# Optimization experiments

Hardware: AMD Instinct MI355X
Metric: run time of the kernel (lower is better)

The kernel has to match this reference:

```python
import math
import jax, jax.numpy as jnp
import numpy as np

B, T, HID = 8, 2048, 1536
H, D = 8, 192
CHUNK, PAST, FUT = 12, 12, 0
CTX = CHUNK + PAST + FUT          # 24
F = PAST + FUT + 1                # 13 relative positions
CAP = 50.0
INVALID = -1.0e9


def setup_inputs() -> dict:
    key = jax.random.key(0)
    k1, k2, k3 = jax.random.split(key, 3)
    x = jax.random.normal(k1, (B, T, HID), dtype=jnp.float32)
    mask = jnp.zeros((B, T), dtype=bool)  # True = invalid/padding
    # causal validity: key offset (c - PAST) relative to query w must lie in [-PAST, FUT]
    w = jnp.arange(CHUNK)[:, None]
    c = jnp.arange(CTX)[None, :]
    causal_valid_mask = (c >= w) & (c <= w + PAST + FUT)  # [CHUNK, CTX]
    W_qkv = jax.random.normal(k2, (HID, 3 * HID), dtype=jnp.float32) * 0.02
    W_pos = jax.random.normal(k3, (HID, HID), dtype=jnp.float32) * 0.02
    per_dim_scale = jnp.zeros((D,), dtype=jnp.float32)
    return {"x": x, "mask": mask, "causal_valid_mask": causal_valid_mask,
            "W_qkv": W_qkv, "W_pos": W_pos, "per_dim_scale": per_dim_scale}


def _extract_block_context(z, U):
    # pad time dim left=PAST, right=FUT+CHUNK-1, then frame with step CHUNK, len CTX
    pad = ((0, 0), (PAST, FUT + CHUNK - 1)) + ((0, 0),) * (z.ndim - 2)
    zp = jnp.pad(z, pad)
    idx = jnp.arange(U)[:, None] * CHUNK + jnp.arange(CTX)[None, :]  # [U, CTX]
    return zp[:, idx]  # [B, U, CTX, ...]


def reference(x, mask, causal_valid_mask, W_qkv, W_pos, per_dim_scale):
    b, t, _ = x.shape
    qkv = x @ W_qkv
    q, k, v = jnp.split(qkv, 3, axis=-1)
    q = q.reshape(b, t, H, D)
    k = k.reshape(b, t, H, D)
    v = v.reshape(b, t, H, D)

    q_scale = D ** (-0.5) / math.log(2.0)
    k_scale = math.log(1.0 + math.e) / math.log(2.0)
    q = q * q_scale * jax.nn.softplus(per_dim_scale)  # per-dim scale on queries
    k = k * k_scale

    U = -(-t // CHUNK)  # ceil
    pad_q = U * CHUNK - t
    qb = jnp.pad(q, ((0, 0), (0, pad_q), (0, 0), (0, 0))).reshape(b, U, CHUNK, H, D)
    kb = _extract_block_context(k, U)            # [B,U,CTX,H,D]
    vb = _extract_block_context(v, U)            # [B,U,CTX,H,D]
    valid = _extract_block_context(~mask, U)     # [B,U,CTX]

    # ---- relative position embedding (Transformer-XL style) ----
    pos = jnp.arange(PAST, -FUT - 1, -1, dtype=jnp.float32)  # [F]
    nts = HID // 2
    inv_ts = jnp.exp(jnp.arange(nts, dtype=jnp.float32) * (-(math.log(10000.0) / (nts - 1))))
    st = pos[:, None] * inv_ts[None, :]
    emb = jnp.concatenate([jnp.sin(st), jnp.cos(st)], axis=-1)  # [F, HID]
    sin_emb = (emb @ W_pos).reshape(F, H, D)

    term_ac = jnp.einsum('buwhd,buchd->bhuwc', qb, kb)     # content-content
    term_bd = jnp.einsum('buwhd,fhd->bhuwf', qb, sin_emb)  # content-position
    # relative shift: pad last dim to CTX+1, flatten, slice, reshape
    pad_amt = CTX + 1 - F
    tb = jnp.pad(term_bd, ((0, 0),) * 4 + ((0, pad_amt),))
    tb = tb.reshape(b, H, U, CHUNK * (CTX + 1))[..., :CHUNK * CTX]
    tb = tb.reshape(b, H, U, CHUNK, CTX)

    logits = term_ac + tb
    logits = jnp.tanh(logits / CAP) * CAP  # softcap
    cond = valid[:, None, :, None, :] & causal_valid_mask[None, None, None, :, :]
    logits = jnp.where(cond, logits, INVALID)
    probs = jax.nn.softmax(logits, axis=-1)
    out = jnp.einsum('bhuwc,buchd->buwhd', probs, vb)
    return out.reshape(b, U * CHUNK, H, D)[:, :t]
```

## Files before the change

kernel.cpp:

```cpp
#include <hip/hip_runtime.h>

typedef unsigned int u32;
typedef unsigned short u16;

typedef __attribute__((ext_vector_type(8))) short bf16x8;
typedef __attribute__((ext_vector_type(4))) float f32x4;

__device__ __forceinline__ u16 f2bf(float f) {
  u32 u = __builtin_bit_cast(u32, f);
  u32 r = (u + 0x7fffu + ((u >> 16) & 1u)) >> 16;
  return (u16)r;
}
__device__ __forceinline__ float bfl(u32 u) { return __builtin_bit_cast(float, u << 16); }
__device__ __forceinline__ float bfh(u32 u) { return __builtin_bit_cast(float, u & 0xffff0000u); }

__device__ __forceinline__ void gload_lds16(const u16* g, u16* l) {
  __builtin_amdgcn_global_load_lds(
      (const __attribute__((address_space(1))) void*)g,
      (__attribute__((address_space(3))) void*)l, 16, 0, 0);
}

__global__ __launch_bounds__(256) void transp_wt(const float* __restrict__ W,
                                                 u16* __restrict__ Wt) {
  __shared__ float tile[64][68];
  int bk = blockIdx.x % 24, bn = blockIdx.x / 24;
  int k0 = bk * 64, n0 = bn * 64;
  int tid = threadIdx.x;
#pragma unroll
  for (int p = 0; p < 4; p++) {
    int idx = p * 256 + tid;
    int r = idx >> 4, c4 = idx & 15;
    *(float4*)&tile[r][c4 * 4] = *(const float4*)&W[(size_t)(k0 + r) * 4608 + n0 + c4 * 4];
  }
  __syncthreads();
#pragma unroll
  for (int p = 0; p < 2; p++) {
    int idx = p * 256 + tid;
    int rn = idx >> 3, kc = idx & 7;
    u16 pk[8];
#pragma unroll
    for (int e = 0; e < 8; e++) pk[e] = f2bf(tile[kc * 8 + e][rn]);
    *(uint4*)&Wt[(size_t)(n0 + rn) * 1536 + k0 + kc * 8] = *(const uint4*)pk;
  }
}

__global__ __launch_bounds__(256) void conv_x(const float* __restrict__ X,
                                              u16* __restrict__ Xb) {
  int i = blockIdx.x * 256 + threadIdx.x;
  const float4* xp = (const float4*)X;
  float4 a = xp[i * 2], b = xp[i * 2 + 1];
  uint4 o;
  o.x = (u32)f2bf(a.x) | ((u32)f2bf(a.y) << 16);
  o.y = (u32)f2bf(a.z) | ((u32)f2bf(a.w) << 16);
  o.z = (u32)f2bf(b.x) | ((u32)f2bf(b.y) << 16);
  o.w = (u32)f2bf(b.z) | ((u32)f2bf(b.w) << 16);
  ((uint4*)Xb)[i] = o;
}

__global__ __launch_bounds__(256) void pos_emb_part(const float* __restrict__ Wp,
                                                    float* __restrict__ part) {
  __shared__ float er[13 * 32];
  int ks = blockIdx.x % 48, nb = blockIdx.x / 48;
  int tid = threadIdx.x;
  int n = nb * 256 + tid;
  const float cfreq = 9.210340371976184f / 767.0f;
  for (int i = tid; i < 13 * 32; i += 256) {
    int f = i >> 5, kk = i & 31;
    int k = ks * 32 + kk;
    int ii = (k < 768) ? k : (k - 768);
    float fr = expf(-cfreq * (float)ii);
    float st = (float)(12 - f) * fr;
    er[f * 32 + kk] = (k < 768) ? sinf(st) : cosf(st);
  }
  __syncthreads();
  float acc[13];
#pragma unroll
  for (int f = 0; f < 13; f++) acc[f] = 0.f;
  const float* wp = Wp + (size_t)(ks * 32) * 1536 + n;
  for (int kk = 0; kk < 32; kk++) {
    float w = wp[(size_t)kk * 1536];
#pragma unroll
    for (int f = 0; f < 13; f++) acc[f] = fmaf(er[f * 32 + kk], w, acc[f]);
  }
#pragma unroll
  for (int f = 0; f < 13; f++)
    part[((size_t)ks * 13 + f) * 1536 + n] = acc[f];
}

__global__ __launch_bounds__(256) void pos_emb_red(const float* __restrict__ part,
                                                   u16* __restrict__ sembbf) {
  int idxg = blockIdx.x * 256 + threadIdx.x;
  int f = idxg / 1536, n = idxg % 1536;
  float s = 0.f;
  if (f < 13)
    for (int ks = 0; ks < 48; ks++)
      s += part[((size_t)ks * 13 + f) * 1536 + n];
  sembbf[idxg] = f2bf(s);
}

__global__ __launch_bounds__(512, 2) void gemm_qkv(const u16* __restrict__ Xb,
                                                   const u16* __restrict__ Bt,
                                                   u16* __restrict__ C,
                                                   const float* __restrict__ pds) {
  extern __shared__ u16 smem[];

  const int tid = threadIdx.x;
  const int lane = tid & 63;
  const int wv = tid >> 6;
  const int wr = wv >> 2;
  const int wc = wv & 3;
  const int lr = lane & 15;
  const int lkq = lane >> 4;
  const int sx = lr & 7;

  int bid = blockIdx.x;
  int xcd = bid & 7, idx = bid >> 3;
  int bm = xcd * 8 + idx / 24;
  int bn = idx % 24;
  int m0 = bm * 256, n0 = bn * 192;

  auto stageA = [&](int T) {
#pragma unroll
    for (int q = 0; q < 4; q++) {
      int ch = q * 512 + tid;
      int r = ch >> 3, cr = ch & 7;
      int crs = cr ^ (r & 7);
      const u16* g = Xb + (size_t)(m0 + r) * 1536 + T * 64 + crs * 8;
      u16* l = smem + (T % 3) * 16384 + ch * 8;
      gload_lds16(g, l);
    }
  };
  auto stageB = [&](int T) {
#pragma unroll
    for (int q = 0; q < 3; q++) {
      int ch = q * 512 + tid;
      int r = ch >> 3, cr = ch & 7;
      int crs = cr ^ (r & 7);
      const u16* g = Bt + (size_t)(n0 + r) * 1536 + T * 64 + crs * 8;
      u16* l = smem + 49152 + (T & 1) * 12288 + ch * 8;
      gload_lds16(g, l);
    }
  };

  f32x4 acc[8][3];
#pragma unroll
  for (int i = 0; i < 8; i++)
#pragma unroll
    for (int j = 0; j < 3; j++) acc[i][j] = (f32x4){0.f, 0.f, 0.f, 0.f};

  stageA(0); stageB(0); stageA(1); stageB(1);
  asm volatile("s_waitcnt vmcnt(7)" ::: "memory");
  __builtin_amdgcn_s_barrier();

  bf16x8 af[8], bfr[6];

  for (int t = 0; t < 24; t++) {
    const int ab = (t % 3) * 16384;
    const int bb = 49152 + (t & 1) * 12288;

#pragma unroll
    for (int j = 0; j < 3; j++)
#pragma unroll
      for (int ks = 0; ks < 2; ks++) {
        int R = wc * 48 + j * 16 + lr;
        bfr[j * 2 + ks] = *(const bf16x8*)&smem[bb + R * 64 + ((ks * 4 + lkq) ^ sx) * 8];
      }
#pragma unroll
    for (int i = 0; i < 4; i++)
#pragma unroll
      for (int ks = 0; ks < 2; ks++) {
        int R = wr * 128 + i * 16 + lr;
        af[i * 2 + ks] = *(const bf16x8*)&smem[ab + R * 64 + ((ks * 4 + lkq) ^ sx) * 8];
      }
    if (t < 22) stageA(t + 2);
    __builtin_amdgcn_s_barrier();
    __builtin_amdgcn_s_setprio(1);
#pragma unroll
    for (int i = 0; i < 4; i++)
#pragma unroll
      for (int j = 0; j < 3; j++)
#pragma unroll
        for (int ks = 0; ks < 2; ks++)
          acc[i][j] = __builtin_amdgcn_mfma_f32_16x16x32_bf16(af[i * 2 + ks], bfr[j * 2 + ks], acc[i][j], 0, 0, 0);
    __builtin_amdgcn_s_setprio(0);
    __builtin_amdgcn_s_barrier();

#pragma unroll
    for (int i = 0; i < 4; i++)
#pragma unroll
      for (int ks = 0; ks < 2; ks++) {
        int R = wr * 128 + 64 + i * 16 + lr;
        af[i * 2 + ks] = *(const bf16x8*)&smem[ab + R * 64 + ((ks * 4 + lkq) ^ sx) * 8];
      }
    if (t < 22) stageB(t + 2);
    __builtin_amdgcn_s_barrier();
    __builtin_amdgcn_s_setprio(1);
#pragma unroll
    for (int i = 0; i < 4; i++)
#pragma unroll
      for (int j = 0; j < 3; j++)
#pragma unroll
        for (int ks = 0; ks < 2; ks++)
          acc[4 + i][j] = __builtin_amdgcn_mfma_f32_16x16x32_bf16(af[i * 2 + ks], bfr[j * 2 + ks], acc[4 + i][j], 0, 0, 0);
    __builtin_amdgcn_s_setprio(0);
    if (t < 22) {
      asm volatile("s_waitcnt vmcnt(7)" ::: "memory");
    } else {
      asm volatile("s_waitcnt vmcnt(0)" ::: "memory");
    }
    __builtin_amdgcn_s_barrier();
  }

  const float kscale = 1.8946361f;
  float scl[3];
#pragma unroll
  for (int j = 0; j < 3; j++) {
    int gcol = n0 + wc * 48 + j * 16 + lr;
    float s;
    if (gcol < 1536) s = 0.10411754f * log1pf(expf(pds[gcol % 192]));
    else if (gcol < 3072) s = kscale;
    else s = 1.0f;
    scl[j] = s;
  }
  int r0 = lkq * 4;
#pragma unroll
  for (int i = 0; i < 8; i++)
#pragma unroll
    for (int j = 0; j < 3; j++) {
      int row = wr * 128 + i * 16 + r0;
      int col = wc * 48 + j * 16 + lr;
#pragma unroll
      for (int r = 0; r < 4; r++)
        smem[(row + r) * 200 + col] = f2bf(acc[i][j][r] * scl[j]);
    }
  asm volatile("s_waitcnt lgkmcnt(0)" ::: "memory");
  __builtin_amdgcn_s_barrier();
#pragma unroll
  for (int p = 0; p < 12; p++) {
    int idx2 = p * 512 + tid;
    int row = idx2 / 24, cq = idx2 % 24;
    *(uint4*)&C[(size_t)(m0 + row) * 4608 + n0 + cq * 8] =
        *(const uint4*)&smem[row * 200 + cq * 8];
  }
}

__global__ __launch_bounds__(512) void qsemb(const u16* __restrict__ qkv,
                                             const u16* __restrict__ sembbf,
                                             float* __restrict__ bdall) {
  int tid = threadIdx.x;
  int lane = tid & 63;
  int h = tid >> 6;
  int t0 = blockIdx.x * 16;
  int arow = lane & 15, ak = lane >> 4;

  const u16* qp = qkv + (size_t)(t0 + arow) * 4608 + h * 192 + ak * 8;
  const u16* sp = sembbf + (size_t)(lane & 15) * 1536 + h * 192 + ak * 8;

  f32x4 acc = (f32x4){0.f, 0.f, 0.f, 0.f};
#pragma unroll
  for (int kt = 0; kt < 6; kt++) {
    bf16x8 a = *(const bf16x8*)(qp + kt * 32);
    bf16x8 bb = *(const bf16x8*)(sp + kt * 32);
    acc = __builtin_amdgcn_mfma_f32_16x16x32_bf16(a, bb, acc, 0, 0, 0);
  }
  int f = lane & 15;
  int rbase = (lane >> 4) * 4;
  if (f < 13) {
#pragma unroll
    for (int r = 0; r < 4; r++)
      bdall[(size_t)(t0 + rbase + r) * 104 + h * 13 + f] = acc[r];
  }
}

__global__ __launch_bounds__(256) void attn_kernel(const u16* __restrict__ qkv,
                                                   const float* __restrict__ bdall,
                                                   const unsigned char* __restrict__ mask,
                                                   float* __restrict__ out) {
  __shared__ u16 sq[24 * 200];
  __shared__ u16 sk[36 * 200];
  __shared__ u16 sv[36 * 200];
  __shared__ float lg[24 * 14];
  __shared__ int vld[36];

  int bid = blockIdx.x;
  int h = bid & 7;
  int u2 = (bid >> 3) % 86;
  int b = bid / (86 * 8);
  int tid = threadIdx.x;
  int tbase = u2 * 24;

  if (tid < 36) {
    int t = tbase + tid - 12;
    vld[tid] = (t >= 0 && t < 2048 && mask[b * 2048 + t] == 0) ? 1 : 0;
  }

  const u16* base = qkv + (size_t)b * 2048 * 4608 + h * 192;
  for (int idx = tid; idx < 576; idx += 256) {
    int w = idx / 24, g = idx % 24;
    int t = tbase + w;
    uint4 val = {0u, 0u, 0u, 0u};
    if (t < 2048) val = *(const uint4*)(base + (size_t)t * 4608 + g * 8);
    *(uint4*)&sq[w * 200 + g * 8] = val;
  }
  for (int idx = tid; idx < 1728; idx += 256) {
    int kv = idx / 864, r = idx % 864;
    int c = r / 24, g = r % 24;
    int t = tbase + c - 12;
    uint4 val = {0u, 0u, 0u, 0u};
    if (t >= 0 && t < 2048)
      val = *(const uint4*)(base + (size_t)t * 4608 + (kv ? 3072 : 1536) + g * 8);
    if (kv) *(uint4*)&sv[c * 200 + g * 8] = val;
    else    *(uint4*)&sk[c * 200 + g * 8] = val;
  }
  __syncthreads();

  for (int idx = tid; idx < 312; idx += 256) {
    int w = idx % 24, f = idx / 24;
    int c = w + f;
    int t = tbase + w;
    float l = -1e9f;
    if (vld[c] && t < 2048) {
      float ac = 0.f;
      const u16* qp = &sq[w * 200];
      const u16* kp = &sk[c * 200];
#pragma unroll 4
      for (int i = 0; i < 24; i++) {
        uint4 qa = *(const uint4*)(qp + i * 8);
        uint4 kb = *(const uint4*)(kp + i * 8);
        ac = fmaf(bfl(qa.x), bfl(kb.x), ac);
        ac = fmaf(bfh(qa.x), bfh(kb.x), ac);
        ac = fmaf(bfl(qa.y), bfl(kb.y), ac);
        ac = fmaf(bfh(qa.y), bfh(kb.y), ac);
        ac = fmaf(bfl(qa.z), bfl(kb.z), ac);
        ac = fmaf(bfh(qa.z), bfh(kb.z), ac);
        ac = fmaf(bfl(qa.w), bfl(kb.w), ac);
        ac = fmaf(bfh(qa.w), bfh(kb.w), ac);
      }
      float bd = bdall[(size_t)(b * 2048 + t) * 104 + h * 13 + f];
      l = tanhf((ac + bd) * 0.02f) * 50.f;
    }
    lg[w * 14 + f] = l;
  }
  __syncthreads();

  if (tid < 24) {
    float m = -3e38f;
#pragma unroll
    for (int f = 0; f < 13; f++) m = fmaxf(m, lg[tid * 14 + f]);
    float s = 0.f;
#pragma unroll
    for (int f = 0; f < 13; f++) {
      float e = expf(lg[tid * 14 + f] - m);
      lg[tid * 14 + f] = e;
      s += e;
    }
    float inv = 1.f / s;
#pragma unroll
    for (int f = 0; f < 13; f++) lg[tid * 14 + f] *= inv;
  }
  __syncthreads();

  for (int idx = tid; idx < 1152; idx += 256) {
    int w = idx / 48, g = idx % 48;
    int t = tbase + w;
    if (t >= 2048) continue;
    float a0 = 0, a1 = 0, a2 = 0, a3 = 0;
#pragma unroll
    for (int f = 0; f < 13; f++) {
      float p = lg[w * 14 + f];
      uint2 vv = *(const uint2*)&sv[(w + f) * 200 + g * 4];
      a0 = fmaf(p, bfl(vv.x), a0);
      a1 = fmaf(p, bfh(vv.x), a1);
      a2 = fmaf(p, bfl(vv.y), a2);
      a3 = fmaf(p, bfh(vv.y), a3);
    }
    float4 o = {a0, a1, a2, a3};
    *(float4*)&out[(((size_t)(b * 2048 + t)) * 8 + h) * 192 + g * 4] = o;
  }
}

extern "C" void kernel_launch(void* const* d_in, const int* in_sizes, int n_in,
                              void* d_out, int out_size, void* d_ws, size_t ws_size,
                              hipStream_t stream) {
  (void)in_sizes; (void)n_in; (void)out_size; (void)ws_size;
  const float* x = (const float*)d_in[0];
  const unsigned char* mask = (const unsigned char*)d_in[1];
  const float* Wqkv = (const float*)d_in[3];
  const float* Wpos = (const float*)d_in[4];
  const float* pds = (const float*)d_in[5];
  float* out = (float*)d_out;

  char* ws = (char*)d_ws;
  u16* Wt = (u16*)ws;
  u16* qkv = (u16*)(ws + 14155776);
  u16* Xb = (u16*)(ws + 165150720);
  u16* sembbf = (u16*)(ws + 215482368);
  float* bdall = (float*)(ws + 215531520);
  float* part = (float*)(ws + 222347264);

  transp_wt<<<1728, 256, 0, stream>>>(Wqkv, Wt);
  conv_x<<<12288, 256, 0, stream>>>(x, Xb);
  pos_emb_part<<<288, 256, 0, stream>>>(Wpos, part);
  pos_emb_red<<<96, 256, 0, stream>>>(part, sembbf);
  gemm_qkv<<<1536, 512, 147456, stream>>>(Xb, Wt, qkv, pds);
  qsemb<<<1024, 512, 0, stream>>>(qkv, sembbf, bdall);
  attn_kernel<<<5504, 256, 0, stream>>>(qkv, bdall, mask, out);
}
```

Baseline: 358.6 us.

## Halve QKV GEMM M-tile to 128 and simplify to double-buffered pipeline

The QKV projection GEMM tile drops from 256x192 to 128x192, so there are twice as many workgroups and each needs less LDS (80 KB instead of 144 KB). The launch-bounds occupancy hint is raised from 2 to 4. The triple-buffered A and split two-phase mainloop become a simple double buffer: the next tile is prefetched at the top of each iteration and followed by a full vmcnt(0) wait and a barrier. The aim is higher occupancy and more parallelism, at the cost of less operand reuse per tile and less latency hiding within each workgroup.

```diff
diff --git a/kernel.cpp b/kernel.cpp
--- a/kernel.cpp
+++ b/kernel.cpp
@@ -98,7 +98,7 @@
   sembbf[idxg] = f2bf(s);
 }
 
-__global__ __launch_bounds__(512, 2) void gemm_qkv(const u16* __restrict__ Xb,
+__global__ __launch_bounds__(512, 4) void gemm_qkv(const u16* __restrict__ Xb,
                                                    const u16* __restrict__ Bt,
                                                    u16* __restrict__ C,
                                                    const float* __restrict__ pds) {
@@ -115,18 +115,18 @@
 
   int bid = blockIdx.x;
   int xcd = bid & 7, idx = bid >> 3;
-  int bm = xcd * 8 + idx / 24;
+  int bm = xcd * 16 + idx / 24;
   int bn = idx % 24;
-  int m0 = bm * 256, n0 = bn * 192;
+  int m0 = bm * 128, n0 = bn * 192;
 
   auto stageA = [&](int T) {
 #pragma unroll
-    for (int q = 0; q < 4; q++) {
+    for (int q = 0; q < 2; q++) {
       int ch = q * 512 + tid;
       int r = ch >> 3, cr = ch & 7;
       int crs = cr ^ (r & 7);
       const u16* g = Xb + (size_t)(m0 + r) * 1536 + T * 64 + crs * 8;
-      u16* l = smem + (T % 3) * 16384 + ch * 8;
+      u16* l = smem + (T & 1) * 8192 + ch * 8;
       gload_lds16(g, l);
     }
   };
@@ -137,26 +137,28 @@
       int r = ch >> 3, cr = ch & 7;
       int crs = cr ^ (r & 7);
       const u16* g = Bt + (size_t)(n0 + r) * 1536 + T * 64 + crs * 8;
-      u16* l = smem + 49152 + (T & 1) * 12288 + ch * 8;
+      u16* l = smem + 16384 + (T & 1) * 12288 + ch * 8;
       gload_lds16(g, l);
     }
   };
 
-  f32x4 acc[8][3];
-#pragma unroll
-  for (int i = 0; i < 8; i++)
+  f32x4 acc[4][3];
+#pragma unroll
+  for (int i = 0; i < 4; i++)
 #pragma unroll
     for (int j = 0; j < 3; j++) acc[i][j] = (f32x4){0.f, 0.f, 0.f, 0.f};
 
-  stageA(0); stageB(0); stageA(1); stageB(1);
-  asm volatile("s_waitcnt vmcnt(7)" ::: "memory");
+  stageA(0); stageB(0);
+  asm volatile("s_waitcnt vmcnt(0)" ::: "memory");
   __builtin_amdgcn_s_barrier();
 
   bf16x8 af[8], bfr[6];
 
   for (int t = 0; t < 24; t++) {
-    const int ab = (t % 3) * 16384;
-    const int bb = 49152 + (t & 1) * 12288;
+    const int ab = (t & 1) * 8192;
+    const int bb = 16384 + (t & 1) * 12288;
+
+    if (t < 23) { stageA(t + 1); stageB(t + 1); }
 
 #pragma unroll
     for (int j = 0; j < 3; j++)
@@ -169,11 +171,10 @@
     for (int i = 0; i < 4; i++)
 #pragma unroll
       for (int ks = 0; ks < 2; ks++) {
-        int R = wr * 128 + i * 16 + lr;
+        int R = wr * 64 + i * 16 + lr;
         af[i * 2 + ks] = *(const bf16x8*)&smem[ab + R * 64 + ((ks * 4 + lkq) ^ sx) * 8];
       }
-    if (t < 22) stageA(t + 2);
-    __builtin_amdgcn_s_barrier();
+
     __builtin_amdgcn_s_setprio(1);
 #pragma unroll
     for (int i = 0; i < 4; i++)
@@ -183,31 +184,8 @@
         for (int ks = 0; ks < 2; ks++)
           acc[i][j] = __builtin_amdgcn_mfma_f32_16x16x32_bf16(af[i * 2 + ks], bfr[j * 2 + ks], acc[i][j], 0, 0, 0);
     __builtin_amdgcn_s_setprio(0);
-    __builtin_amdgcn_s_barrier();
-
-#pragma unroll
-    for (int i = 0; i < 4; i++)
-#pragma unroll
-      for (int ks = 0; ks < 2; ks++) {
-        int R = wr * 128 + 64 + i * 16 + lr;
-        af[i * 2 + ks] = *(const bf16x8*)&smem[ab + R * 64 + ((ks * 4 + lkq) ^ sx) * 8];
-      }
-    if (t < 22) stageB(t + 2);
-    __builtin_amdgcn_s_barrier();
-    __builtin_amdgcn_s_setprio(1);
-#pragma unroll
-    for (int i = 0; i < 4; i++)
-#pragma unroll
-      for (int j = 0; j < 3; j++)
-#pragma unroll
-        for (int ks = 0; ks < 2; ks++)
-          acc[4 + i][j] = __builtin_amdgcn_mfma_f32_16x16x32_bf16(af[i * 2 + ks], bfr[j * 2 + ks], acc[4 + i][j], 0, 0, 0);
-    __builtin_amdgcn_s_setprio(0);
-    if (t < 22) {
-      asm volatile("s_waitcnt vmcnt(7)" ::: "memory");
-    } else {
-      asm volatile("s_waitcnt vmcnt(0)" ::: "memory");
-    }
+
+    asm volatile("s_waitcnt vmcnt(0)" ::: "memory");
     __builtin_amdgcn_s_barrier();
   }
 
@@ -224,10 +202,10 @@
   }
   int r0 = lkq * 4;
 #pragma unroll
-  for (int i = 0; i < 8; i++)
+  for (int i = 0; i < 4; i++)
 #pragma unroll
     for (int j = 0; j < 3; j++) {
-      int row = wr * 128 + i * 16 + r0;
+      int row = wr * 64 + i * 16 + r0;
       int col = wc * 48 + j * 16 + lr;
 #pragma unroll
       for (int r = 0; r < 4; r++)
@@ -236,7 +214,7 @@
   asm volatile("s_waitcnt lgkmcnt(0)" ::: "memory");
   __builtin_amdgcn_s_barrier();
 #pragma unroll
-  for (int p = 0; p < 12; p++) {
+  for (int p = 0; p < 6; p++) {
     int idx2 = p * 512 + tid;
     int row = idx2 / 24, cq = idx2 % 24;
     *(uint4*)&C[(size_t)(m0 + row) * 4608 + n0 + cq * 8] =
@@ -402,7 +380,7 @@
   conv_x<<<12288, 256, 0, stream>>>(x, Xb);
   pos_emb_part<<<288, 256, 0, stream>>>(Wpos, part);
   pos_emb_red<<<96, 256, 0, stream>>>(part, sembbf);
-  gemm_qkv<<<1536, 512, 147456, stream>>>(Xb, Wt, qkv, pds);
+  gemm_qkv<<<3072, 512, 81920, stream>>>(Xb, Wt, qkv, pds);
   qsemb<<<1024, 512, 0, stream>>>(qkv, sembbf, bdall);
   attn_kernel<<<5504, 256, 0, stream>>>(qkv, bdall, mask, out);
 }
```

After: 380.8 us. 1.06x slower.
